# Kernel optimization log

Measured on AMD Instinct MI355X. Metric: run time of the kernel, lower is better.

Reference implementation:

```python
import jax, jax.numpy as jnp
import numpy as np

N = 131072   # nodes (flattened batch)
SI, VI = 128, 64   # in_dims
SO, VO = 128, 64   # out_dims
HD = 128           # h_dim


def setup_inputs() -> dict:
    key = jax.random.key(0)
    ks = jax.random.split(key, 8)
    scale = lambda fan_in: 1.0 / np.sqrt(fan_in)
    return {
        "s": jax.random.normal(ks[0], (N, SI), dtype=jnp.float32),
        "V": jax.random.normal(ks[1], (N, VI, 3), dtype=jnp.float32),
        # Linear(vi, h_dim, bias=False): weight [h_dim, vi]
        "W_h": jax.random.uniform(ks[2], (HD, VI), jnp.float32, -scale(VI), scale(VI)),
        # Linear(h_dim, vo, bias=False): weight [vo, h_dim]
        "W_V": jax.random.uniform(ks[3], (VO, HD), jnp.float32, -scale(HD), scale(HD)),
        # Linear(si + h_dim, so)
        "W_s_w": jax.random.uniform(ks[4], (SO, SI + HD), jnp.float32, -scale(SI + HD), scale(SI + HD)),
        "W_s_b": jax.random.uniform(ks[5], (SO,), jnp.float32, -scale(SI + HD), scale(SI + HD)),
        # Linear(so, vo) gate
        "W_g_w": jax.random.uniform(ks[6], (VO, SO), jnp.float32, -scale(SO), scale(SO)),
        "W_g_b": jax.random.uniform(ks[7], (VO,), jnp.float32, -scale(SO), scale(SO)),
    }


def reference(s, V, W_h, W_V, W_s_w, W_s_b, W_g_w, W_g_b):
    # Vh: contract vector-channel dim vi, keep 3 spatial dims -> [N, h_dim, 3]
    Vh = jnp.einsum("nvc,hv->nhc", V, W_h)
    # L2 norm over the 3 spatial dims -> [N, h_dim]
    Vh_norm = jnp.sqrt(jnp.sum(Vh * Vh, axis=-1))
    # V_out: [N, vo, 3]
    V_out = jnp.einsum("nhc,oh->noc", Vh, W_V)
    # scalar path: concat + linear + relu -> [N, so]
    s_cat = jnp.concatenate([s, Vh_norm], axis=-1)
    s_out = jax.nn.relu(s_cat @ W_s_w.T + W_s_b)
    # vector gate: sigmoid(Linear(s_out)) broadcast over spatial dim
    gate = jax.nn.sigmoid(s_out @ W_g_w.T + W_g_b)[..., None]  # [N, vo, 1]
    V_out = V_out * gate
    return s_out, V_out
```

## Files before the change

kernel.cpp:

```cpp
#include <hip/hip_runtime.h>
#include <hip/hip_bf16.h>
#include <math.h>

#define NNODES 131072
#define BN 64

typedef __attribute__((ext_vector_type(8))) short bf16x8;
typedef __attribute__((ext_vector_type(4))) float f32x4;

__device__ short g_w[49152];
__device__ short g_wc[4096];

__device__ __forceinline__ short f2b(float f) {
  union { float f; unsigned u; } x; x.f = f;
  unsigned r = x.u + 0x7fffu + ((x.u >> 16) & 1u);
  return (short)(r >> 16);
}
__device__ __forceinline__ short c2b(float f) {
  __hip_bfloat16 h = __float2bfloat16(f);
  return *reinterpret_cast<short*>(&h);
}

__global__ void prep_kernel(const float* __restrict__ W_h, const float* __restrict__ W_V,
                            const float* __restrict__ W_s_w, const float* __restrict__ W_g_w) {
  int b = blockIdx.x;
  if (b < 48) {
    int i4 = (b * 256 + threadIdx.x) * 4;
    const float* src;
    if (i4 < 8192)       src = W_h   + i4;
    else if (i4 < 40960) src = W_s_w + (i4 - 8192);
    else                 src = W_g_w + (i4 - 40960);
    float4 q = *(const float4*)src;
    short4 p;
    p.x = f2b(q.x); p.y = f2b(q.y); p.z = f2b(q.z); p.w = f2b(q.w);
    *(short4*)(g_w + i4) = p;
  } else {
    int gid = (b - 48) * 256 + threadIdx.x;
    int o  = gid >> 4;
    int v0 = (gid & 15) * 4;
    float a0 = 0.f, a1 = 0.f, a2 = 0.f, a3 = 0.f;
    #pragma unroll 8
    for (int h = 0; h < 128; ++h) {
      float wv = W_V[o * 128 + h];
      float4 wh = *(const float4*)(W_h + h * 64 + v0);
      a0 += wv * wh.x; a1 += wv * wh.y; a2 += wv * wh.z; a3 += wv * wh.w;
    }
    short4 p;
    p.x = f2b(a0); p.y = f2b(a1); p.z = f2b(a2); p.w = f2b(a3);
    *(short4*)(g_wc + o * 64 + v0) = p;
  }
}


__global__ __launch_bounds__(512, 2)
void gvp_kernel(const float* __restrict__ s_in, const float* __restrict__ V_in,
                const float* __restrict__ W_s_b, const float* __restrict__ W_g_b,
                float* __restrict__ s_out_g, float* __restrict__ V_out_g)
{
  __shared__ __align__(16) char smem[57344];
  char*  const Vt   = smem;
  float* const VST  = (float*)smem;
  char*  const SCN  = smem + 24576;
  char*  const SOUT = smem + 24576;

  const short* const g_wh = g_w;
  const short* const g_ws = g_w + 8192;
  const short* const g_wg = g_w + 40960;

  const int t    = threadIdx.x;
  const int lane = t & 63;
  const int w    = t >> 6;
  const int w4   = w & 3;
  const int h2   = w >> 2;
  const int l15  = lane & 15;
  const int lk8  = (lane >> 4) << 3;
  const int r4   = (lane >> 4) << 2;
  const long n0  = (long)blockIdx.x * BN;

  {
    const int nl = t >> 3;
    const int vg = t & 7;
    const int v0 = vg << 3;
    const float* vp = V_in + (n0 + nl) * 192 + v0 * 3;
    float fl[24];
    #pragma unroll
    for (int i = 0; i < 6; ++i) *(float4*)(fl + 4 * i) = *(const float4*)(vp + 4 * i);
    #pragma unroll
    for (int c = 0; c < 3; ++c) {
      int row = (c << 6) + nl;
      bf16x8 p;
      #pragma unroll
      for (int j = 0; j < 8; ++j) p[j] = c2b(fl[j * 3 + c]);
      unsigned a = (unsigned)(row * 128) + (((unsigned)(v0 * 2)) ^ (unsigned)((row & 7) << 4));
      *(bf16x8*)(Vt + a) = p;
    }
  }
  {
    const int nl = t >> 3;
    const int kg = t & 7;
    const int k0 = kg << 4;
    const float* sp = s_in + (n0 + nl) * 128 + k0;
    float4 q0 = *(const float4*)(sp);
    float4 q1 = *(const float4*)(sp + 4);
    float4 q2 = *(const float4*)(sp + 8);
    float4 q3 = *(const float4*)(sp + 12);
    bf16x8 pa, pb;
    pa[0] = c2b(q0.x); pa[1] = c2b(q0.y); pa[2] = c2b(q0.z); pa[3] = c2b(q0.w);
    pa[4] = c2b(q1.x); pa[5] = c2b(q1.y); pa[6] = c2b(q1.z); pa[7] = c2b(q1.w);
    pb[0] = c2b(q2.x); pb[1] = c2b(q2.y); pb[2] = c2b(q2.z); pb[3] = c2b(q2.w);
    pb[4] = c2b(q3.x); pb[5] = c2b(q3.y); pb[6] = c2b(q3.z); pb[7] = c2b(q3.w);
    unsigned sw = (unsigned)((nl & 7) << 4);
    *(bf16x8*)(SCN + nl * 512 + (((unsigned)(k0 * 2)) ^ sw))      = pa;
    *(bf16x8*)(SCN + nl * 512 + (((unsigned)(k0 * 2 + 16)) ^ sw)) = pb;
  }
  __syncthreads();

  bf16x8 bf1[2];
  {
    int h = (w << 4) + l15;
    bf1[0] = *(const bf16x8*)(g_wh + h * 64 + lk8);
    bf1[1] = *(const bf16x8*)(g_wh + h * 64 + 32 + lk8);
  }
  bf16x8 b3[8];
  {
    int o = (w << 4) + l15;
    #pragma unroll
    for (int ks = 0; ks < 8; ++ks)
      b3[ks] = *(const bf16x8*)(g_ws + o * 256 + (ks << 5) + lk8);
  }
  bf16x8 bc[2];
  {
    int o = (w4 << 4) + l15;
    bc[0] = *(const bf16x8*)(g_wc + o * 64 + lk8);
    bc[1] = *(const bf16x8*)(g_wc + o * 64 + 32 + lk8);
  }

  f32x4 acc1[12];
  #pragma unroll
  for (int r = 0; r < 12; ++r) { f32x4 z = {0.f,0.f,0.f,0.f}; acc1[r] = z; }
  #pragma unroll
  for (int r = 0; r < 12; ++r) {
    int row = (r << 4) + l15;
    unsigned sw = (unsigned)((row & 7) << 4);
    bf16x8 af0 = *(const bf16x8*)(Vt + row * 128 + (((unsigned)(lk8 * 2)) ^ sw));
    bf16x8 af1 = *(const bf16x8*)(Vt + row * 128 + (((unsigned)((32 + lk8) * 2)) ^ sw));
    acc1[r] = __builtin_amdgcn_mfma_f32_16x16x32_bf16(af0, bf1[0], acc1[r], 0, 0, 0);
    acc1[r] = __builtin_amdgcn_mfma_f32_16x16x32_bf16(af1, bf1[1], acc1[r], 0, 0, 0);
  }

  {
    int col = 128 + (w << 4) + l15;
    #pragma unroll
    for (int q = 0; q < 4; ++q) {
      #pragma unroll
      for (int i = 0; i < 4; ++i) {
        int nl = (q << 4) + r4 + i;
        float x0 = acc1[q][i];
        float x1 = acc1[4 + q][i];
        float x2 = acc1[8 + q][i];
        float nrm = sqrtf(x0 * x0 + x1 * x1 + x2 * x2);
        unsigned a = (unsigned)(nl * 512) + (((unsigned)(col * 2)) ^ (unsigned)((nl & 7) << 4));
        *(short*)(SCN + a) = c2b(nrm);
      }
    }
  }
  __syncthreads();

  bf16x8 b4[4];
  {
    int o = (w4 << 4) + l15;
    #pragma unroll
    for (int ks = 0; ks < 4; ++ks)
      b4[ks] = *(const bf16x8*)(g_wg + o * 128 + (ks << 5) + lk8);
  }

  f32x4 acc3[4];
  #pragma unroll
  for (int rt = 0; rt < 4; ++rt) { f32x4 z = {0.f,0.f,0.f,0.f}; acc3[rt] = z; }
  #pragma unroll
  for (int ks = 0; ks < 8; ++ks) {
    #pragma unroll
    for (int rt = 0; rt < 4; ++rt) {
      int row = (rt << 4) + l15;
      unsigned sw = (unsigned)((row & 7) << 4);
      bf16x8 a = *(const bf16x8*)(SCN + row * 512 +
                   (((unsigned)(((ks << 5) + lk8) * 2)) ^ sw));
      acc3[rt] = __builtin_amdgcn_mfma_f32_16x16x32_bf16(a, b3[ks], acc3[rt], 0, 0, 0);
    }
  }

  f32x4 acc2[3][2];
  #pragma unroll
  for (int c = 0; c < 3; ++c)
    #pragma unroll
    for (int j = 0; j < 2; ++j) { f32x4 z = {0.f,0.f,0.f,0.f}; acc2[c][j] = z; }
  #pragma unroll
  for (int c = 0; c < 3; ++c) {
    #pragma unroll
    for (int j = 0; j < 2; ++j) {
      int r = c * 4 + 2 * h2 + j;
      int row = (r << 4) + l15;
      unsigned sw = (unsigned)((row & 7) << 4);
      bf16x8 af0 = *(const bf16x8*)(Vt + row * 128 + (((unsigned)(lk8 * 2)) ^ sw));
      bf16x8 af1 = *(const bf16x8*)(Vt + row * 128 + (((unsigned)((32 + lk8) * 2)) ^ sw));
      acc2[c][j] = __builtin_amdgcn_mfma_f32_16x16x32_bf16(af0, bc[0], acc2[c][j], 0, 0, 0);
      acc2[c][j] = __builtin_amdgcn_mfma_f32_16x16x32_bf16(af1, bc[1], acc2[c][j], 0, 0, 0);
    }
  }

  float so[4][4];
  {
    float bias = W_s_b[(w << 4) + l15];
    #pragma unroll
    for (int rt = 0; rt < 4; ++rt)
      #pragma unroll
      for (int i = 0; i < 4; ++i)
        so[rt][i] = fmaxf(acc3[rt][i] + bias, 0.0f);
  }
  __syncthreads();

  {
    int col = (w << 4) + l15;
    #pragma unroll
    for (int rt = 0; rt < 4; ++rt) {
      #pragma unroll
      for (int i = 0; i < 4; ++i) {
        int row = (rt << 4) + r4 + i;
        unsigned a = (unsigned)(row * 256) + (((unsigned)(col * 2)) ^ (unsigned)((row & 7) << 4));
        *(short*)(SOUT + a) = c2b(so[rt][i]);
      }
    }
  }
  __syncthreads();

  f32x4 acc4[2];
  { f32x4 z = {0.f,0.f,0.f,0.f}; acc4[0] = z; acc4[1] = z; }
  #pragma unroll
  for (int ks = 0; ks < 4; ++ks) {
    #pragma unroll
    for (int j = 0; j < 2; ++j) {
      int row = ((2 * h2 + j) << 4) + l15;
      bf16x8 a = *(const bf16x8*)(SOUT + row * 256 +
                   (((unsigned)(((ks << 5) + lk8) * 2)) ^ ((unsigned)((row & 7) << 4))));
      acc4[j] = __builtin_amdgcn_mfma_f32_16x16x32_bf16(a, b4[ks], acc4[j], 0, 0, 0);
    }
  }
  float sg[2][4];
  {
    float biasg = W_g_b[(w4 << 4) + l15];
    #pragma unroll
    for (int j = 0; j < 2; ++j)
      #pragma unroll
      for (int i = 0; i < 4; ++i)
        sg[j][i] = 1.0f / (1.0f + __expf(-(acc4[j][i] + biasg)));
  }
  __syncthreads();

  {
    int col = (w4 << 4) + l15;
    #pragma unroll
    for (int c = 0; c < 3; ++c) {
      #pragma unroll
      for (int j = 0; j < 2; ++j) {
        #pragma unroll
        for (int i = 0; i < 4; ++i) {
          int nl = ((2 * h2 + j) << 4) + r4 + i;
          unsigned a = (unsigned)(nl * 768) +
                       (((unsigned)((col * 3 + c) * 4)) ^ (unsigned)((nl & 7) << 4));
          *(float*)((char*)VST + a) = acc2[c][j][i] * sg[j][i];
        }
      }
    }
  }
  __syncthreads();

  {
    float4* Vo = (float4*)(V_out_g + n0 * 192);
    #pragma unroll
    for (int m = 0; m < 6; ++m) {
      int f = m * 512 + t;
      int nl = f / 48;
      int rem = f - nl * 48;
      float4 q = *(const float4*)((char*)VST + nl * 768 +
                   (((unsigned)(rem * 16)) ^ ((unsigned)((nl & 7) << 4))));
      Vo[f] = q;
    }
  }
  {
    int col = (w << 4) + l15;
    #pragma unroll
    for (int rt = 0; rt < 4; ++rt) {
      #pragma unroll
      for (int i = 0; i < 4; ++i) {
        int nl = (rt << 4) + r4 + i;
        s_out_g[(n0 + nl) * 128 + col] = so[rt][i];
      }
    }
  }
}

extern "C" void kernel_launch(void* const* d_in, const int* in_sizes, int n_in,
                              void* d_out, int out_size, void* d_ws, size_t ws_size,
                              hipStream_t stream) {
  const float* s_in  = (const float*)d_in[0];
  const float* V_in  = (const float*)d_in[1];
  const float* W_h   = (const float*)d_in[2];
  const float* W_V   = (const float*)d_in[3];
  const float* W_s_w = (const float*)d_in[4];
  const float* W_s_b = (const float*)d_in[5];
  const float* W_g_w = (const float*)d_in[6];
  const float* W_g_b = (const float*)d_in[7];
  float* out = (float*)d_out;
  float* s_out_g = out;
  float* V_out_g = out + (size_t)NNODES * 128;
  hipLaunchKernelGGL(prep_kernel, dim3(52), dim3(256), 0, stream,
                     W_h, W_V, W_s_w, W_g_w);
  hipLaunchKernelGGL(gvp_kernel, dim3(NNODES / BN), dim3(512), 0, stream,
                     s_in, V_in, W_s_b, W_g_b, s_out_g, V_out_g);
}
```

Baseline: 94.88 us.

## Process two node tiles per block with register prefetch of next tile

Each block now handles two 64-node tiles in a loop, halving the grid. The inputs for the next tile are loaded into registers right after the first barrier, so those global reads can overlap the current tile's MFMA work. The cost is higher register pressure, possibly lower occupancy, and fewer blocks to spread across the CUs.

```diff
diff --git a/kernel.cpp b/kernel.cpp
--- a/kernel.cpp
+++ b/kernel.cpp
@@ -4,6 +4,7 @@
 
 #define NNODES 131072
 #define BN 64
+#define TILES 2
 
 typedef __attribute__((ext_vector_type(8))) short bf16x8;
 typedef __attribute__((ext_vector_type(4))) float f32x4;
@@ -75,227 +76,245 @@
   const int l15  = lane & 15;
   const int lk8  = (lane >> 4) << 3;
   const int r4   = (lane >> 4) << 2;
-  const long n0  = (long)blockIdx.x * BN;
-
+  const long base = (long)blockIdx.x * (BN * TILES);
+
+  const int snl = t >> 3;
+  const int svg = t & 7;
+  const int sv0 = svg << 3;
+  const int sk0 = svg << 4;
+
+  float4 vr[6], sr[4];
   {
-    const int nl = t >> 3;
-    const int vg = t & 7;
-    const int v0 = vg << 3;
-    const float* vp = V_in + (n0 + nl) * 192 + v0 * 3;
-    float fl[24];
-    #pragma unroll
-    for (int i = 0; i < 6; ++i) *(float4*)(fl + 4 * i) = *(const float4*)(vp + 4 * i);
-    #pragma unroll
-    for (int c = 0; c < 3; ++c) {
-      int row = (c << 6) + nl;
-      bf16x8 p;
-      #pragma unroll
-      for (int j = 0; j < 8; ++j) p[j] = c2b(fl[j * 3 + c]);
-      unsigned a = (unsigned)(row * 128) + (((unsigned)(v0 * 2)) ^ (unsigned)((row & 7) << 4));
-      *(bf16x8*)(Vt + a) = p;
-    }
+    const float* vp = V_in + (base + snl) * 192 + sv0 * 3;
+    #pragma unroll
+    for (int i = 0; i < 6; ++i) vr[i] = *(const float4*)(vp + 4 * i);
+    const float* sp = s_in + (base + snl) * 128 + sk0;
+    #pragma unroll
+    for (int i = 0; i < 4; ++i) sr[i] = *(const float4*)(sp + 4 * i);
   }
-  {
-    const int nl = t >> 3;
-    const int kg = t & 7;
-    const int k0 = kg << 4;
-    const float* sp = s_in + (n0 + nl) * 128 + k0;
-    float4 q0 = *(const float4*)(sp);
-    float4 q1 = *(const float4*)(sp + 4);
-    float4 q2 = *(const float4*)(sp + 8);
-    float4 q3 = *(const float4*)(sp + 12);
-    bf16x8 pa, pb;
-    pa[0] = c2b(q0.x); pa[1] = c2b(q0.y); pa[2] = c2b(q0.z); pa[3] = c2b(q0.w);
-    pa[4] = c2b(q1.x); pa[5] = c2b(q1.y); pa[6] = c2b(q1.z); pa[7] = c2b(q1.w);
-    pb[0] = c2b(q2.x); pb[1] = c2b(q2.y); pb[2] = c2b(q2.z); pb[3] = c2b(q2.w);
-    pb[4] = c2b(q3.x); pb[5] = c2b(q3.y); pb[6] = c2b(q3.z); pb[7] = c2b(q3.w);
-    unsigned sw = (unsigned)((nl & 7) << 4);
-    *(bf16x8*)(SCN + nl * 512 + (((unsigned)(k0 * 2)) ^ sw))      = pa;
-    *(bf16x8*)(SCN + nl * 512 + (((unsigned)(k0 * 2 + 16)) ^ sw)) = pb;
-  }
-  __syncthreads();
-
-  bf16x8 bf1[2];
-  {
-    int h = (w << 4) + l15;
-    bf1[0] = *(const bf16x8*)(g_wh + h * 64 + lk8);
-    bf1[1] = *(const bf16x8*)(g_wh + h * 64 + 32 + lk8);
-  }
-  bf16x8 b3[8];
-  {
-    int o = (w << 4) + l15;
-    #pragma unroll
-    for (int ks = 0; ks < 8; ++ks)
-      b3[ks] = *(const bf16x8*)(g_ws + o * 256 + (ks << 5) + lk8);
-  }
-  bf16x8 bc[2];
-  {
-    int o = (w4 << 4) + l15;
-    bc[0] = *(const bf16x8*)(g_wc + o * 64 + lk8);
-    bc[1] = *(const bf16x8*)(g_wc + o * 64 + 32 + lk8);
-  }
-
-  f32x4 acc1[12];
+
   #pragma unroll
-  for (int r = 0; r < 12; ++r) { f32x4 z = {0.f,0.f,0.f,0.f}; acc1[r] = z; }
-  #pragma unroll
-  for (int r = 0; r < 12; ++r) {
-    int row = (r << 4) + l15;
-    unsigned sw = (unsigned)((row & 7) << 4);
-    bf16x8 af0 = *(const bf16x8*)(Vt + row * 128 + (((unsigned)(lk8 * 2)) ^ sw));
-    bf16x8 af1 = *(const bf16x8*)(Vt + row * 128 + (((unsigned)((32 + lk8) * 2)) ^ sw));
-    acc1[r] = __builtin_amdgcn_mfma_f32_16x16x32_bf16(af0, bf1[0], acc1[r], 0, 0, 0);
-    acc1[r] = __builtin_amdgcn_mfma_f32_16x16x32_bf16(af1, bf1[1], acc1[r], 0, 0, 0);
-  }
-
-  {
-    int col = 128 + (w << 4) + l15;
-    #pragma unroll
-    for (int q = 0; q < 4; ++q) {
-      #pragma unroll
-      for (int i = 0; i < 4; ++i) {
-        int nl = (q << 4) + r4 + i;
-        float x0 = acc1[q][i];
-        float x1 = acc1[4 + q][i];
-        float x2 = acc1[8 + q][i];
-        float nrm = sqrtf(x0 * x0 + x1 * x1 + x2 * x2);
-        unsigned a = (unsigned)(nl * 512) + (((unsigned)(col * 2)) ^ (unsigned)((nl & 7) << 4));
-        *(short*)(SCN + a) = c2b(nrm);
-      }
-    }
-  }
-  __syncthreads();
-
-  bf16x8 b4[4];
-  {
-    int o = (w4 << 4) + l15;
-    #pragma unroll
-    for (int ks = 0; ks < 4; ++ks)
-      b4[ks] = *(const bf16x8*)(g_wg + o * 128 + (ks << 5) + lk8);
-  }
-
-  f32x4 acc3[4];
-  #pragma unroll
-  for (int rt = 0; rt < 4; ++rt) { f32x4 z = {0.f,0.f,0.f,0.f}; acc3[rt] = z; }
-  #pragma unroll
-  for (int ks = 0; ks < 8; ++ks) {
-    #pragma unroll
-    for (int rt = 0; rt < 4; ++rt) {
-      int row = (rt << 4) + l15;
-      unsigned sw = (unsigned)((row & 7) << 4);
-      bf16x8 a = *(const bf16x8*)(SCN + row * 512 +
-                   (((unsigned)(((ks << 5) + lk8) * 2)) ^ sw));
-      acc3[rt] = __builtin_amdgcn_mfma_f32_16x16x32_bf16(a, b3[ks], acc3[rt], 0, 0, 0);
-    }
-  }
-
-  f32x4 acc2[3][2];
-  #pragma unroll
-  for (int c = 0; c < 3; ++c)
-    #pragma unroll
-    for (int j = 0; j < 2; ++j) { f32x4 z = {0.f,0.f,0.f,0.f}; acc2[c][j] = z; }
-  #pragma unroll
-  for (int c = 0; c < 3; ++c) {
-    #pragma unroll
-    for (int j = 0; j < 2; ++j) {
-      int r = c * 4 + 2 * h2 + j;
+  for (int tt = 0; tt < TILES; ++tt) {
+    const long n0 = base + (long)tt * BN;
+
+    {
+      float fl[24];
+      #pragma unroll
+      for (int i = 0; i < 6; ++i) *(float4*)(fl + 4 * i) = vr[i];
+      #pragma unroll
+      for (int c = 0; c < 3; ++c) {
+        int row = (c << 6) + snl;
+        bf16x8 p;
+        #pragma unroll
+        for (int j = 0; j < 8; ++j) p[j] = c2b(fl[j * 3 + c]);
+        unsigned a = (unsigned)(row * 128) + (((unsigned)(sv0 * 2)) ^ (unsigned)((row & 7) << 4));
+        *(bf16x8*)(Vt + a) = p;
+      }
+    }
+    {
+      bf16x8 pa, pb;
+      pa[0] = c2b(sr[0].x); pa[1] = c2b(sr[0].y); pa[2] = c2b(sr[0].z); pa[3] = c2b(sr[0].w);
+      pa[4] = c2b(sr[1].x); pa[5] = c2b(sr[1].y); pa[6] = c2b(sr[1].z); pa[7] = c2b(sr[1].w);
+      pb[0] = c2b(sr[2].x); pb[1] = c2b(sr[2].y); pb[2] = c2b(sr[2].z); pb[3] = c2b(sr[2].w);
+      pb[4] = c2b(sr[3].x); pb[5] = c2b(sr[3].y); pb[6] = c2b(sr[3].z); pb[7] = c2b(sr[3].w);
+      unsigned sw = (unsigned)((snl & 7) << 4);
+      *(bf16x8*)(SCN + snl * 512 + (((unsigned)(sk0 * 2)) ^ sw))      = pa;
+      *(bf16x8*)(SCN + snl * 512 + (((unsigned)(sk0 * 2 + 16)) ^ sw)) = pb;
+    }
+    __syncthreads();
+
+    if (tt + 1 < TILES) {
+      const float* vp = V_in + (n0 + BN + snl) * 192 + sv0 * 3;
+      #pragma unroll
+      for (int i = 0; i < 6; ++i) vr[i] = *(const float4*)(vp + 4 * i);
+      const float* sp = s_in + (n0 + BN + snl) * 128 + sk0;
+      #pragma unroll
+      for (int i = 0; i < 4; ++i) sr[i] = *(const float4*)(sp + 4 * i);
+    }
+
+    bf16x8 bf1[2];
+    {
+      int h = (w << 4) + l15;
+      bf1[0] = *(const bf16x8*)(g_wh + h * 64 + lk8);
+      bf1[1] = *(const bf16x8*)(g_wh + h * 64 + 32 + lk8);
+    }
+    bf16x8 b3[8];
+    {
+      int o = (w << 4) + l15;
+      #pragma unroll
+      for (int ks = 0; ks < 8; ++ks)
+        b3[ks] = *(const bf16x8*)(g_ws + o * 256 + (ks << 5) + lk8);
+    }
+    bf16x8 bc[2];
+    {
+      int o = (w4 << 4) + l15;
+      bc[0] = *(const bf16x8*)(g_wc + o * 64 + lk8);
+      bc[1] = *(const bf16x8*)(g_wc + o * 64 + 32 + lk8);
+    }
+
+    f32x4 acc1[12];
+    #pragma unroll
+    for (int r = 0; r < 12; ++r) { f32x4 z = {0.f,0.f,0.f,0.f}; acc1[r] = z; }
+    #pragma unroll
+    for (int r = 0; r < 12; ++r) {
       int row = (r << 4) + l15;
       unsigned sw = (unsigned)((row & 7) << 4);
       bf16x8 af0 = *(const bf16x8*)(Vt + row * 128 + (((unsigned)(lk8 * 2)) ^ sw));
       bf16x8 af1 = *(const bf16x8*)(Vt + row * 128 + (((unsigned)((32 + lk8) * 2)) ^ sw));
-      acc2[c][j] = __builtin_amdgcn_mfma_f32_16x16x32_bf16(af0, bc[0], acc2[c][j], 0, 0, 0);
-      acc2[c][j] = __builtin_amdgcn_mfma_f32_16x16x32_bf16(af1, bc[1], acc2[c][j], 0, 0, 0);
-    }
-  }
-
-  float so[4][4];
-  {
-    float bias = W_s_b[(w << 4) + l15];
-    #pragma unroll
-    for (int rt = 0; rt < 4; ++rt)
-      #pragma unroll
-      for (int i = 0; i < 4; ++i)
-        so[rt][i] = fmaxf(acc3[rt][i] + bias, 0.0f);
-  }
-  __syncthreads();
-
-  {
-    int col = (w << 4) + l15;
-    #pragma unroll
-    for (int rt = 0; rt < 4; ++rt) {
-      #pragma unroll
-      for (int i = 0; i < 4; ++i) {
-        int row = (rt << 4) + r4 + i;
-        unsigned a = (unsigned)(row * 256) + (((unsigned)(col * 2)) ^ (unsigned)((row & 7) << 4));
-        *(short*)(SOUT + a) = c2b(so[rt][i]);
-      }
-    }
-  }
-  __syncthreads();
-
-  f32x4 acc4[2];
-  { f32x4 z = {0.f,0.f,0.f,0.f}; acc4[0] = z; acc4[1] = z; }
-  #pragma unroll
-  for (int ks = 0; ks < 4; ++ks) {
-    #pragma unroll
-    for (int j = 0; j < 2; ++j) {
-      int row = ((2 * h2 + j) << 4) + l15;
-      bf16x8 a = *(const bf16x8*)(SOUT + row * 256 +
-                   (((unsigned)(((ks << 5) + lk8) * 2)) ^ ((unsigned)((row & 7) << 4))));
-      acc4[j] = __builtin_amdgcn_mfma_f32_16x16x32_bf16(a, b4[ks], acc4[j], 0, 0, 0);
-    }
-  }
-  float sg[2][4];
-  {
-    float biasg = W_g_b[(w4 << 4) + l15];
-    #pragma unroll
-    for (int j = 0; j < 2; ++j)
-      #pragma unroll
-      for (int i = 0; i < 4; ++i)
-        sg[j][i] = 1.0f / (1.0f + __expf(-(acc4[j][i] + biasg)));
-  }
-  __syncthreads();
-
-  {
-    int col = (w4 << 4) + l15;
+      acc1[r] = __builtin_amdgcn_mfma_f32_16x16x32_bf16(af0, bf1[0], acc1[r], 0, 0, 0);
+      acc1[r] = __builtin_amdgcn_mfma_f32_16x16x32_bf16(af1, bf1[1], acc1[r], 0, 0, 0);
+    }
+
+    {
+      int col = 128 + (w << 4) + l15;
+      #pragma unroll
+      for (int q = 0; q < 4; ++q) {
+        #pragma unroll
+        for (int i = 0; i < 4; ++i) {
+          int nl = (q << 4) + r4 + i;
+          float x0 = acc1[q][i];
+          float x1 = acc1[4 + q][i];
+          float x2 = acc1[8 + q][i];
+          float nrm = sqrtf(x0 * x0 + x1 * x1 + x2 * x2);
+          unsigned a = (unsigned)(nl * 512) + (((unsigned)(col * 2)) ^ (unsigned)((nl & 7) << 4));
+          *(short*)(SCN + a) = c2b(nrm);
+        }
+      }
+    }
+    __syncthreads();
+
+    bf16x8 b4[4];
+    {
+      int o = (w4 << 4) + l15;
+      #pragma unroll
+      for (int ks = 0; ks < 4; ++ks)
+        b4[ks] = *(const bf16x8*)(g_wg + o * 128 + (ks << 5) + lk8);
+    }
+
+    f32x4 acc3[4];
+    #pragma unroll
+    for (int rt = 0; rt < 4; ++rt) { f32x4 z = {0.f,0.f,0.f,0.f}; acc3[rt] = z; }
+    #pragma unroll
+    for (int ks = 0; ks < 8; ++ks) {
+      #pragma unroll
+      for (int rt = 0; rt < 4; ++rt) {
+        int row = (rt << 4) + l15;
+        unsigned sw = (unsigned)((row & 7) << 4);
+        bf16x8 a = *(const bf16x8*)(SCN + row * 512 +
+                     (((unsigned)(((ks << 5) + lk8) * 2)) ^ sw));
+        acc3[rt] = __builtin_amdgcn_mfma_f32_16x16x32_bf16(a, b3[ks], acc3[rt], 0, 0, 0);
+      }
+    }
+
+    f32x4 acc2[3][2];
+    #pragma unroll
+    for (int c = 0; c < 3; ++c)
+      #pragma unroll
+      for (int j = 0; j < 2; ++j) { f32x4 z = {0.f,0.f,0.f,0.f}; acc2[c][j] = z; }
     #pragma unroll
     for (int c = 0; c < 3; ++c) {
       #pragma unroll
       for (int j = 0; j < 2; ++j) {
+        int r = c * 4 + 2 * h2 + j;
+        int row = (r << 4) + l15;
+        unsigned sw = (unsigned)((row & 7) << 4);
+        bf16x8 af0 = *(const bf16x8*)(Vt + row * 128 + (((unsigned)(lk8 * 2)) ^ sw));
+        bf16x8 af1 = *(const bf16x8*)(Vt + row * 128 + (((unsigned)((32 + lk8) * 2)) ^ sw));
+        acc2[c][j] = __builtin_amdgcn_mfma_f32_16x16x32_bf16(af0, bc[0], acc2[c][j], 0, 0, 0);
+        acc2[c][j] = __builtin_amdgcn_mfma_f32_16x16x32_bf16(af1, bc[1], acc2[c][j], 0, 0, 0);
+      }
+    }
+
+    float so[4][4];
+    {
+      float bias = W_s_b[(w << 4) + l15];
+      #pragma unroll
+      for (int rt = 0; rt < 4; ++rt)
+        #pragma unroll
+        for (int i = 0; i < 4; ++i)
+          so[rt][i] = fmaxf(acc3[rt][i] + bias, 0.0f);
+    }
+    __syncthreads();
+
+    {
+      int col = (w << 4) + l15;
+      #pragma unroll
+      for (int rt = 0; rt < 4; ++rt) {
         #pragma unroll
         for (int i = 0; i < 4; ++i) {
-          int nl = ((2 * h2 + j) << 4) + r4 + i;
-          unsigned a = (unsigned)(nl * 768) +
-                       (((unsigned)((col * 3 + c) * 4)) ^ (unsigned)((nl & 7) << 4));
-          *(float*)((char*)VST + a) = acc2[c][j][i] * sg[j][i];
+          int row = (rt << 4) + r4 + i;
+          unsigned a = (unsigned)(row * 256) + (((unsigned)(col * 2)) ^ (unsigned)((row & 7) << 4));
+          *(short*)(SOUT + a) = c2b(so[rt][i]);
         }
       }
     }
-  }
-  __syncthreads();
-
-  {
-    float4* Vo = (float4*)(V_out_g + n0 * 192);
-    #pragma unroll
-    for (int m = 0; m < 6; ++m) {
-      int f = m * 512 + t;
-      int nl = f / 48;
-      int rem = f - nl * 48;
-      float4 q = *(const float4*)((char*)VST + nl * 768 +
-                   (((unsigned)(rem * 16)) ^ ((unsigned)((nl & 7) << 4))));
-      Vo[f] = q;
-    }
-  }
-  {
-    int col = (w << 4) + l15;
-    #pragma unroll
-    for (int rt = 0; rt < 4; ++rt) {
-      #pragma unroll
-      for (int i = 0; i < 4; ++i) {
-        int nl = (rt << 4) + r4 + i;
-        s_out_g[(n0 + nl) * 128 + col] = so[rt][i];
-      }
-    }
+    __syncthreads();
+
+    f32x4 acc4[2];
+    { f32x4 z = {0.f,0.f,0.f,0.f}; acc4[0] = z; acc4[1] = z; }
+    #pragma unroll
+    for (int ks = 0; ks < 4; ++ks) {
+      #pragma unroll
+      for (int j = 0; j < 2; ++j) {
+        int row = ((2 * h2 + j) << 4) + l15;
+        bf16x8 a = *(const bf16x8*)(SOUT + row * 256 +
+                     (((unsigned)(((ks << 5) + lk8) * 2)) ^ ((unsigned)((row & 7) << 4))));
+        acc4[j] = __builtin_amdgcn_mfma_f32_16x16x32_bf16(a, b4[ks], acc4[j], 0, 0, 0);
+      }
+    }
+    float sg[2][4];
+    {
+      float biasg = W_g_b[(w4 << 4) + l15];
+      #pragma unroll
+      for (int j = 0; j < 2; ++j)
+        #pragma unroll
+        for (int i = 0; i < 4; ++i)
+          sg[j][i] = 1.0f / (1.0f + __expf(-(acc4[j][i] + biasg)));
+    }
+    __syncthreads();
+
+    {
+      int col = (w4 << 4) + l15;
+      #pragma unroll
+      for (int c = 0; c < 3; ++c) {
+        #pragma unroll
+        for (int j = 0; j < 2; ++j) {
+          #pragma unroll
+          for (int i = 0; i < 4; ++i) {
+            int nl = ((2 * h2 + j) << 4) + r4 + i;
+            unsigned a = (unsigned)(nl * 768) +
+                         (((unsigned)((col * 3 + c) * 4)) ^ (unsigned)((nl & 7) << 4));
+            *(float*)((char*)VST + a) = acc2[c][j][i] * sg[j][i];
+          }
+        }
+      }
+    }
+    __syncthreads();
+
+    {
+      float4* Vo = (float4*)(V_out_g + n0 * 192);
+      #pragma unroll
+      for (int m = 0; m < 6; ++m) {
+        int f = m * 512 + t;
+        int nl = f / 48;
+        int rem = f - nl * 48;
+        float4 q = *(const float4*)((char*)VST + nl * 768 +
+                     (((unsigned)(rem * 16)) ^ ((unsigned)((nl & 7) << 4))));
+        Vo[f] = q;
+      }
+    }
+    {
+      int col = (w << 4) + l15;
+      #pragma unroll
+      for (int rt = 0; rt < 4; ++rt) {
+        #pragma unroll
+        for (int i = 0; i < 4; ++i) {
+          int nl = (rt << 4) + r4 + i;
+          s_out_g[(n0 + nl) * 128 + col] = so[rt][i];
+        }
+      }
+    }
+    if (tt + 1 < TILES) __syncthreads();
   }
 }
 
@@ -315,6 +334,6 @@
   float* V_out_g = out + (size_t)NNODES * 128;
   hipLaunchKernelGGL(prep_kernel, dim3(52), dim3(256), 0, stream,
                      W_h, W_V, W_s_w, W_g_w);
-  hipLaunchKernelGGL(gvp_kernel, dim3(NNODES / BN), dim3(512), 0, stream,
+  hipLaunchKernelGGL(gvp_kernel, dim3(NNODES / (BN * TILES)), dim3(512), 0, stream,
                      s_in, V_in, W_s_b, W_g_b, s_out_g, V_out_g);
 }
```

Measured after the change: 112.1 us. +18.1%, slower.
